# Optimization experiments

Measured on AMD Instinct MI355X. Metric: run time of the kernel, lower is better.

Reference implementation:

```python
import jax, jax.numpy as jnp
import numpy as np

N_FULL, N_LOCAL, N_GLOBAL = 6, 4, 2
N_HEADS = N_FULL + N_LOCAL + N_GLOBAL
WINDOW = 64
DIM = 1536
B, S = 2, 2048


def setup_inputs() -> dict:
    key = jax.random.key(0)
    k0, k1, k2 = jax.random.split(key, 3)
    sc = DIM ** -0.5
    return {
        "x": jax.random.normal(k0, (B, S, DIM), dtype=jnp.float32),
        "Wqkv": jax.random.normal(k1, (DIM, 3 * DIM), dtype=jnp.float32) * sc,
        "bqkv": jnp.zeros((3 * DIM,), dtype=jnp.float32),
        "Wout": jax.random.normal(k2, (DIM, DIM), dtype=jnp.float32) * sc,
        "bout": jnp.zeros((DIM,), dtype=jnp.float32),
    }


def _attend(q, k, v, scale, bias=None):
    # q,k,v: [B,H,S,D]
    scores = jnp.einsum("bhqd,bhkd->bhqk", q, k) * scale
    if bias is not None:
        scores = scores + bias
    p = jax.nn.softmax(scores, axis=-1)
    return jnp.einsum("bhqk,bhkd->bhqd", p, v)


def reference(x, Wqkv, bqkv, Wout, bout):
    Bb, Ss, D = x.shape
    hd = D // N_HEADS
    scale = hd ** -0.5
    qkv = (x @ Wqkv + bqkv).reshape(Bb, Ss, 3, N_HEADS, hd)
    qkv = jnp.transpose(qkv, (2, 0, 3, 1, 4))  # [3,B,H,S,hd]
    q, k, v = qkv[0], qkv[1], qkv[2]
    h1 = N_FULL
    h2 = N_FULL + N_LOCAL

    # tier 1: full attention on first n_full heads
    out_full = _attend(q[:, :h1], k[:, :h1], v[:, :h1], scale)

    # tier 2: sliding-window (|i-j| <= window//2 allowed) on next n_local heads
    idx = jnp.arange(Ss)
    allowed = jnp.abs(idx[:, None] - idx[None, :]) <= WINDOW // 2  # [S,S]
    bias = jnp.where(allowed, 0.0, -jnp.inf).astype(x.dtype)[None, None]
    out_local = _attend(q[:, h1:h2], k[:, h1:h2], v[:, h1:h2], scale, bias)

    # tier 3: global — attend only to first and last tokens
    kg = jnp.stack([k[:, h2:, 0], k[:, h2:, -1]], axis=2)  # [B,Hg,2,hd]
    vg = jnp.stack([v[:, h2:, 0], v[:, h2:, -1]], axis=2)
    out_global = _attend(q[:, h2:], kg, vg, scale)

    out = jnp.concatenate([out_full, out_local, out_global], axis=1)  # [B,H,S,hd]
    out = jnp.transpose(out, (0, 2, 1, 3)).reshape(Bb, Ss, D)
    return out @ Wout + bout
```

## Files before the change

### kernel.cpp

```cpp
#include <hip/hip_runtime.h>
#include <hip/hip_bf16.h>

#define SEQ    2048
#define TOK    4096
#define DMODEL 1536
#define QKVROW 4608
#define HD     128
#define SCALE  0.08838834764831845f

#define NSPLIT 4
#define KRANGE (SEQ / NSPLIT)
#define NPAIR  12
#define ROWS_P (NPAIR * SEQ)
#define OPART_ELEMS ((size_t)ROWS_P * HD)

typedef __attribute__((ext_vector_type(8))) short short8;
typedef __attribute__((ext_vector_type(4))) short short4v;
typedef __attribute__((ext_vector_type(4))) float f32x4;

__device__ __forceinline__ float b2f(short s) {
    union { unsigned u; float f; } x;
    x.u = ((unsigned)(unsigned short)s) << 16;
    return x.f;
}
__device__ __forceinline__ short f2b(float f) {
    union { float f; unsigned u; } x; x.f = f;
    unsigned u = x.u;
    unsigned r = (u + 0x7fffu + ((u >> 16) & 1u)) >> 16;
    return (short)r;
}

__device__ __forceinline__ void gld_lds16(const short* g, short* l) {
    __builtin_amdgcn_global_load_lds(
        (__attribute__((address_space(1))) void*)(g),
        (__attribute__((address_space(3))) void*)(l), 16, 0, 0);
}

#define CVT_BLOCKS  6144
#define TQKV_BLOCKS 1728
#define TOUT_BLOCKS 576

__device__ __forceinline__ void transpose_tile(
    const float* __restrict__ W, short* __restrict__ WT,
    int K, int N, int k0, int n0, int t, short (*tile)[65])
{
    {
        int j  = t & 63;
        int i0 = (t >> 6) * 16;
        for (int ii = 0; ii < 16; ++ii)
            tile[i0 + ii][j] = f2b(W[(size_t)(k0 + i0 + ii) * N + n0 + j]);
    }
    __syncthreads();
    {
        int i  = t & 63;
        int j0 = (t >> 6) * 16;
        for (int jj = 0; jj < 16; ++jj)
            WT[(size_t)(n0 + j0 + jj) * K + k0 + i] = tile[i][j0 + jj];
    }
}

__global__ __launch_bounds__(256) void prepass_k(
    const float* __restrict__ x, const float* __restrict__ Wqkv,
    const float* __restrict__ Wout, short* __restrict__ xb,
    short* __restrict__ WqkvT, short* __restrict__ WoutT)
{
    __shared__ short tile[64][65];
    const int bid = blockIdx.x;
    const int t   = threadIdx.x;
    if (bid < CVT_BLOCKS) {
        int i = bid * 1024 + t * 4;
        float4 v = *(const float4*)(x + i);
        short4v b = { f2b(v.x), f2b(v.y), f2b(v.z), f2b(v.w) };
        *(short4v*)(xb + i) = b;
    } else if (bid < CVT_BLOCKS + TQKV_BLOCKS) {
        int tb = bid - CVT_BLOCKS;
        transpose_tile(Wqkv, WqkvT, DMODEL, QKVROW,
                       (tb / (QKVROW / 64)) * 64, (tb % (QKVROW / 64)) * 64, t, tile);
    } else {
        int tb = bid - (CVT_BLOCKS + TQKV_BLOCKS);
        transpose_tile(Wout, WoutT, DMODEL, DMODEL,
                       (tb / (DMODEL / 64)) * 64, (tb % (DMODEL / 64)) * 64, t, tile);
    }
}

__device__ __forceinline__ short* ldsA(short* s, int slot, int kh, int st) {
    return s + ((slot * 2 + kh) * 8 + st) * 512;
}
__device__ __forceinline__ short* ldsB(short* s, int slot, int kh, int st) {
    return s + 16384 + ((slot * 2 + kh) * 16 + st) * 512;
}

template <int SLOT, int KH, int G>
__device__ __forceinline__ void ld_a(short8 af[2], short* smem, int wm4, int lane) {
#pragma unroll
    for (int mi = 0; mi < 2; ++mi)
        af[mi] = *(const short8*)(ldsA(smem, SLOT, KH, wm4 + G * 2 + mi) + lane * 8);
}
template <int SLOT, int KH>
__device__ __forceinline__ void ld_b(short8 bf[4], short* smem, int wn4, int lane) {
#pragma unroll
    for (int ni = 0; ni < 4; ++ni)
        bf[ni] = *(const short8*)(ldsB(smem, SLOT, KH, wn4 + ni) + lane * 8);
}
template <int G>
__device__ __forceinline__ void mfma8(f32x4 (&acc)[4][4], const short8 af[2], const short8 bf[4]) {
#pragma unroll
    for (int mi = 0; mi < 2; ++mi)
#pragma unroll
        for (int ni = 0; ni < 4; ++ni)
            acc[G * 2 + mi][ni] = __builtin_amdgcn_mfma_f32_16x16x32_bf16(
                af[mi], bf[ni], acc[G * 2 + mi][ni], 0, 0, 0);
}

#define STG_A(S, KH, KT) gld_lds16(gA0 + (KT) * 64 + (KH) * 32, ldsA(smem, (S), (KH), wave))
#define STG_B(S, KH, KT)                                                        \
    do {                                                                        \
        gld_lds16(gB0 + (KT) * 64 + (KH) * 32, ldsB(smem, (S), (KH), wave));    \
        gld_lds16(gB1 + (KT) * 64 + (KH) * 32, ldsB(smem, (S), (KH), 8 + wave));\
    } while (0)

#define PH(S, KH, G, LOADB, STG_STMT, VMW)                          \
    do {                                                            \
        ld_a<S, KH, G>(af, smem, wm4, lane);                        \
        if (LOADB) ld_b<S, KH>(bf, smem, wn4, lane);                \
        STG_STMT;                                                   \
        asm volatile("" ::: "memory");                              \
        __builtin_amdgcn_s_barrier();                               \
        asm volatile("s_waitcnt lgkmcnt(0)" ::: "memory");          \
        __builtin_amdgcn_s_setprio(1);                              \
        mfma8<G>(acc, af, bf);                                      \
        __builtin_amdgcn_s_setprio(0);                              \
        if (VMW) asm volatile("s_waitcnt vmcnt(5)" ::: "memory");   \
        asm volatile("" ::: "memory");                              \
        __builtin_amdgcn_s_barrier();                               \
        asm volatile("" ::: "memory");                              \
    } while (0)

template <bool OUT_BF16, int MT, int NT>
__global__ __launch_bounds__(512, 2) void gemm128x256_8ph(
    const short* __restrict__ A, const short* __restrict__ BT,
    const float* __restrict__ bias, void* __restrict__ Cout,
    int N, int K)
{
    __shared__ short smem[49152];

    constexpr int NWG = MT * NT;
    constexpr int Q8  = NWG / 8, R8 = NWG % 8;
    constexpr int BW  = 4;
    constexpr int FULLB = NT / BW;
    constexpr int TB  = FULLB * MT * BW;
    constexpr int TW  = NT - FULLB * BW;
    const int orig = blockIdx.x;
    const int xcd  = orig & 7, idx = orig >> 3;
    const int wg   = (xcd < R8 ? xcd * (Q8 + 1) : R8 * (Q8 + 1) + (xcd - R8) * Q8) + idx;
    int mt, nt;
    if (TW == 0 || wg < TB) {
        int band = wg / (MT * BW);
        int rem  = wg % (MT * BW);
        mt = rem / BW;
        nt = band * BW + rem % BW;
    } else {
        constexpr int TWD = TW ? TW : 1;
        int rem = wg - TB;
        mt = rem / TWD;
        nt = FULLB * BW + rem % TWD;
    }
    const int bm0 = mt * 128;
    const int bn0 = nt * 256;

    const int t    = threadIdx.x;
    const int wave = t >> 6;
    const int lane = t & 63;
    const int quad = lane >> 4;
    const int lo   = lane & 15;
    const int wm   = wave >> 2;
    const int wn   = wave & 3;
    const int wm4  = wm * 4;
    const int wn4  = wn * 4;

    const int rO = quad * 8;
    const short* gA0 = A  + (size_t)(bm0 + wave * 16 + lo) * K + rO;
    const short* gB0 = BT + (size_t)(bn0 + wave * 16 + lo) * K + rO;
    const short* gB1 = BT + (size_t)(bn0 + (8 + wave) * 16 + lo) * K + rO;

    f32x4 acc[4][4];
#pragma unroll
    for (int i = 0; i < 4; ++i)
#pragma unroll
        for (int j = 0; j < 4; ++j)
            acc[i][j] = (f32x4){0.f, 0.f, 0.f, 0.f};

    const int NTK = K >> 6;

    STG_A(0, 0, 0); STG_A(0, 1, 0); STG_B(0, 0, 0); STG_B(0, 1, 0);
    STG_B(1, 0, 1); STG_A(1, 0, 1); STG_B(1, 1, 1);
    asm volatile("s_waitcnt vmcnt(5)" ::: "memory");
    asm volatile("" ::: "memory");
    __builtin_amdgcn_s_barrier();
    asm volatile("" ::: "memory");

    short8 af[2], bf[4];
#pragma unroll 1
    for (int it = 0; it < (NTK >> 1); ++it) {
        const int T  = it * 2;
        const int t2 = min(T + 2, NTK - 1);
        const int t3 = min(T + 3, NTK - 1);
        PH(0, 0, 0, true,  STG_A(1, 1, T + 1), 0);
        PH(0, 0, 1, false, STG_B(0, 0, t2),    0);
        PH(0, 1, 0, true,  STG_A(0, 0, t2),    0);
        PH(0, 1, 1, false, STG_B(0, 1, t2),    1);
        PH(1, 0, 0, true,  STG_A(0, 1, t2),    0);
        PH(1, 0, 1, false, STG_B(1, 0, t3),    0);
        PH(1, 1, 0, true,  STG_A(1, 0, t3),    0);
        PH(1, 1, 1, false, STG_B(1, 1, t3),    1);
    }
    asm volatile("s_waitcnt vmcnt(0)" ::: "memory");

#pragma unroll
    for (int ni = 0; ni < 4; ++ni) {
        int col  = bn0 + wn * 64 + ni * 16 + lo;
        float bv = bias[col];
#pragma unroll
        for (int mi = 0; mi < 4; ++mi)
#pragma unroll
            for (int r = 0; r < 4; ++r) {
                int row   = bm0 + wm * 64 + mi * 16 + quad * 4 + r;
                float val = acc[mi][ni][r] + bv;
                if (OUT_BF16)
                    ((short*)Cout)[(size_t)row * N + col] = f2b(val);
                else
                    ((float*)Cout)[(size_t)row * N + col] = val;
            }
    }
}

#define KSP 136
#define VTP 44
#define PLP 40

__global__ __launch_bounds__(256) void attn_full_split(
    const short* __restrict__ qkv, short* __restrict__ Opart,
    float* __restrict__ lsum)
{
    const int pair = blockIdx.y;
    const int b    = pair / 6;
    const int h    = pair % 6;
    const int q0   = blockIdx.x * 64;
    const int kz   = blockIdx.z;
    const int t    = threadIdx.x;
    const int wave = t >> 6;
    const int lane = t & 63;
    const int quad = lane >> 4;
    const int lo   = lane & 15;

    __shared__ short Ks[32 * KSP];
    __shared__ short Vr[32 * KSP];
    __shared__ short Vt[128 * VTP];
    __shared__ short Pl[4][16 * PLP];

    const short* base = qkv + (size_t)b * SEQ * QKVROW;

    short8 qf[4];
    {
        int qrow = q0 + wave * 16 + lo;
        const short* qp = base + (size_t)qrow * QKVROW + h * HD;
        for (int c = 0; c < 4; ++c)
            qf[c] = *(const short8*)(qp + c * 32 + quad * 8);
    }

    f32x4 o[8];
    for (int i = 0; i < 8; ++i) o[i] = (f32x4){0.f, 0.f, 0.f, 0.f};
    float lrow[4] = {0.f, 0.f, 0.f, 0.f};

    const int skey = t >> 3;
    const int sdc  = (t & 7) * 16;
    const int thd  = t & 127;
    const int tkc  = (t >> 7) * 16;

    const int kend = kz * KRANGE + KRANGE;
    for (int k0 = kz * KRANGE; k0 < kend; k0 += 32) {
        {
            const short* kro = base + (size_t)(k0 + skey) * QKVROW + DMODEL     + h * HD + sdc;
            const short* vro = base + (size_t)(k0 + skey) * QKVROW + 2 * DMODEL + h * HD + sdc;
            short8 ka = *(const short8*)kro;
            short8 kb = *(const short8*)(kro + 8);
            short8 va = *(const short8*)vro;
            short8 vb = *(const short8*)(vro + 8);
            *(short8*)(Ks + skey * KSP + sdc)     = ka;
            *(short8*)(Ks + skey * KSP + sdc + 8) = kb;
            *(short8*)(Vr + skey * KSP + sdc)     = va;
            *(short8*)(Vr + skey * KSP + sdc + 8) = vb;
        }
        __syncthreads();

        {
            short8 x0, x1;
            for (int j = 0; j < 8; ++j) x0[j] = Vr[(tkc + j) * KSP + thd];
            for (int j = 0; j < 8; ++j) x1[j] = Vr[(tkc + 8 + j) * KSP + thd];
            *(short8*)(Vt + thd * VTP + tkc)     = x0;
            *(short8*)(Vt + thd * VTP + tkc + 8) = x1;
        }

        f32x4 s[2];
        s[0] = (f32x4){0.f, 0.f, 0.f, 0.f};
        s[1] = (f32x4){0.f, 0.f, 0.f, 0.f};
        for (int g = 0; g < 2; ++g)
            for (int c = 0; c < 4; ++c) {
                short8 kf = *(const short8*)(Ks + (g * 16 + lo) * KSP + c * 32 + quad * 8);
                s[g] = __builtin_amdgcn_mfma_f32_16x16x32_bf16(qf[c], kf, s[g], 0, 0, 0);
            }

        for (int g = 0; g < 2; ++g)
            for (int r = 0; r < 4; ++r) {
                float p = __expf(s[g][r] * SCALE);
                lrow[r] += p;
                Pl[wave][(quad * 4 + r) * PLP + g * 16 + lo] = f2b(p);
            }
        __syncthreads();

        short8 pf = *(const short8*)(&Pl[wave][lo * PLP + quad * 8]);
        for (int ni = 0; ni < 8; ++ni) {
            short8 vf = *(const short8*)(Vt + (ni * 16 + lo) * VTP + quad * 8);
            o[ni] = __builtin_amdgcn_mfma_f32_16x16x32_bf16(pf, vf, o[ni], 0, 0, 0);
        }
    }

    for (int r = 0; r < 4; ++r)
        for (int off = 1; off < 16; off <<= 1)
            lrow[r] += __shfl_xor(lrow[r], off, 64);

    for (int ni = 0; ni < 8; ++ni)
        for (int r = 0; r < 4; ++r) {
            int grow = pair * SEQ + q0 + wave * 16 + quad * 4 + r;
            Opart[(size_t)kz * OPART_ELEMS + (size_t)grow * HD + ni * 16 + lo] =
                f2b(o[ni][r]);
        }
    if (lo == 0)
        for (int r = 0; r < 4; ++r) {
            int grow = pair * SEQ + q0 + wave * 16 + quad * 4 + r;
            lsum[kz * ROWS_P + grow] = lrow[r];
        }
}

__global__ __launch_bounds__(256) void attn_local_mfma(
    const short* __restrict__ qkv, short* __restrict__ att)
{
    const int pair = blockIdx.y;
    const int b    = pair >> 2;
    const int h    = 6 + (pair & 3);
    const int q0   = blockIdx.x * 64;
    const int t    = threadIdx.x;
    const int wave = t >> 6;
    const int lane = t & 63;
    const int quad = lane >> 4;
    const int lo   = lane & 15;

    __shared__ short Ks[32 * KSP];
    __shared__ short Vr[32 * KSP];
    __shared__ short Vt[128 * VTP];
    __shared__ short Pl[4][16 * PLP];

    const short* base = qkv + (size_t)b * SEQ * QKVROW;

    short8 qf[4];
    {
        int qrow = q0 + wave * 16 + lo;
        const short* qp = base + (size_t)qrow * QKVROW + h * HD;
        for (int c = 0; c < 4; ++c)
            qf[c] = *(const short8*)(qp + c * 32 + quad * 8);
    }

    f32x4 o[8];
    for (int i = 0; i < 8; ++i) o[i] = (f32x4){0.f, 0.f, 0.f, 0.f};
    float lrow[4] = {0.f, 0.f, 0.f, 0.f};

    const int skey = t >> 3;
    const int sdc  = (t & 7) * 16;
    const int thd  = t & 127;
    const int tkc  = (t >> 7) * 16;
    const int irow = q0 + wave * 16 + quad * 4;

    const int ks = max(0, q0 - 32);
    const int ke = min(SEQ, q0 + 96);
    for (int k0 = ks; k0 < ke; k0 += 32) {
        {
            const short* kro = base + (size_t)(k0 + skey) * QKVROW + DMODEL     + h * HD + sdc;
            const short* vro = base + (size_t)(k0 + skey) * QKVROW + 2 * DMODEL + h * HD + sdc;
            short8 ka = *(const short8*)kro;
            short8 kb = *(const short8*)(kro + 8);
            short8 va = *(const short8*)vro;
            short8 vb = *(const short8*)(vro + 8);
            *(short8*)(Ks + skey * KSP + sdc)     = ka;
            *(short8*)(Ks + skey * KSP + sdc + 8) = kb;
            *(short8*)(Vr + skey * KSP + sdc)     = va;
            *(short8*)(Vr + skey * KSP + sdc + 8) = vb;
        }
        __syncthreads();

        {
            short8 x0, x1;
            for (int j = 0; j < 8; ++j) x0[j] = Vr[(tkc + j) * KSP + thd];
            for (int j = 0; j < 8; ++j) x1[j] = Vr[(tkc + 8 + j) * KSP + thd];
            *(short8*)(Vt + thd * VTP + tkc)     = x0;
            *(short8*)(Vt + thd * VTP + tkc + 8) = x1;
        }

        f32x4 s[2];
        s[0] = (f32x4){0.f, 0.f, 0.f, 0.f};
        s[1] = (f32x4){0.f, 0.f, 0.f, 0.f};
        for (int g = 0; g < 2; ++g)
            for (int c = 0; c < 4; ++c) {
                short8 kf = *(const short8*)(Ks + (g * 16 + lo) * KSP + c * 32 + quad * 8);
                s[g] = __builtin_amdgcn_mfma_f32_16x16x32_bf16(qf[c], kf, s[g], 0, 0, 0);
            }

        for (int g = 0; g < 2; ++g)
            for (int r = 0; r < 4; ++r) {
                int j = k0 + g * 16 + lo;
                int d = irow + r - j;
                float p = (d >= -32 && d <= 32) ? __expf(s[g][r] * SCALE) : 0.f;
                lrow[r] += p;
                Pl[wave][(quad * 4 + r) * PLP + g * 16 + lo] = f2b(p);
            }
        __syncthreads();

        short8 pf = *(const short8*)(&Pl[wave][lo * PLP + quad * 8]);
        for (int ni = 0; ni < 8; ++ni) {
            short8 vf = *(const short8*)(Vt + (ni * 16 + lo) * VTP + quad * 8);
            o[ni] = __builtin_amdgcn_mfma_f32_16x16x32_bf16(pf, vf, o[ni], 0, 0, 0);
        }
    }

    for (int r = 0; r < 4; ++r)
        for (int off = 1; off < 16; off <<= 1)
            lrow[r] += __shfl_xor(lrow[r], off, 64);

    for (int ni = 0; ni < 8; ++ni)
        for (int r = 0; r < 4; ++r) {
            int row = irow + r;
            size_t off = ((size_t)(b * SEQ + row)) * DMODEL + h * HD + ni * 16 + lo;
            att[off] = f2b(o[ni][r] / lrow[r]);
        }
}

#define MERGE_BLOCKS  12288
#define GLOBAL_BLOCKS 2048

__global__ __launch_bounds__(256) void postattn_k(
    const short* __restrict__ qkv, const short* __restrict__ Opart,
    const float* __restrict__ lsum, short* __restrict__ att)
{
    const int bid  = blockIdx.x;
    const int t    = threadIdx.x;
    const int wave = t >> 6;
    const int lane = t & 63;

    if (bid < MERGE_BLOCKS) {
        int idx  = bid * 256 + t;
        int pair = idx >> 18;
        int q    = (idx >> 7) & (SEQ - 1);
        int hd   = idx & (HD - 1);
        int row  = pair * SEQ + q;
        float osum = 0.f, ls = 0.f;
        for (int z = 0; z < NSPLIT; ++z) {
            ls   += lsum[z * ROWS_P + row];
            osum += b2f(Opart[(size_t)z * OPART_ELEMS + (size_t)row * HD + hd]);
        }
        int b = pair / 6, h = pair % 6;
        att[((size_t)(b * SEQ + q)) * DMODEL + h * HD + hd] = f2b(osum / ls);
    } else {
        int gb   = bid - MERGE_BLOCKS;
        int pair = gb >> 9;
        int q    = (gb & 511) * 4 + wave;
        int b    = pair >> 1;
        int h    = 10 + (pair & 1);

        const short* base = qkv + (size_t)b * SEQ * QKVROW;
        const short* qp   = base + (size_t)q * QKVROW + h * HD;
        const short* k0   = base + DMODEL + h * HD;
        const short* k1   = base + (size_t)(SEQ - 1) * QKVROW + DMODEL + h * HD;

        float s0 = fmaf(b2f(qp[lane]), b2f(k0[lane]),
                   b2f(qp[lane + 64]) * b2f(k0[lane + 64]));
        float s1 = fmaf(b2f(qp[lane]), b2f(k1[lane]),
                   b2f(qp[lane + 64]) * b2f(k1[lane + 64]));
        for (int off = 1; off < 64; off <<= 1) {
            s0 += __shfl_xor(s0, off, 64);
            s1 += __shfl_xor(s1, off, 64);
        }
        s0 *= SCALE; s1 *= SCALE;
        float m  = fmaxf(s0, s1);
        float e0 = __expf(s0 - m), e1 = __expf(s1 - m);
        float inv = 1.f / (e0 + e1);
        float p0 = e0 * inv, p1 = e1 * inv;

        const short* v0 = base + 2 * DMODEL + h * HD;
        const short* v1 = base + (size_t)(SEQ - 1) * QKVROW + 2 * DMODEL + h * HD;
        size_t ob = ((size_t)(b * SEQ + q)) * DMODEL + h * HD;
        att[ob + lane]      = f2b(fmaf(p0, b2f(v0[lane]),      p1 * b2f(v1[lane])));
        att[ob + lane + 64] = f2b(fmaf(p0, b2f(v0[lane + 64]), p1 * b2f(v1[lane + 64])));
    }
}

extern "C" void kernel_launch(void* const* d_in, const int* in_sizes, int n_in,
                              void* d_out, int out_size, void* d_ws, size_t ws_size,
                              hipStream_t stream) {
    const float* x    = (const float*)d_in[0];
    const float* Wqkv = (const float*)d_in[1];
    const float* bqkv = (const float*)d_in[2];
    const float* Wout = (const float*)d_in[3];
    const float* bout = (const float*)d_in[4];

    char* p = (char*)d_ws;
    short* qkv   = (short*)p;  p += (size_t)TOK * QKVROW * 2;
    short* Opart = (short*)p;  p += OPART_ELEMS * NSPLIT * 2;
    float* lsum  = (float*)p;  p += (size_t)ROWS_P * NSPLIT * 4;
    short* xb    = (short*)p;  p += (size_t)TOK * DMODEL * 2;
    short* att   = xb;
    short* WqkvT = (short*)p;  p += (size_t)QKVROW * DMODEL * 2;
    short* WoutT = (short*)p;

    prepass_k<<<dim3(CVT_BLOCKS + TQKV_BLOCKS + TOUT_BLOCKS), 256, 0, stream>>>(
        x, Wqkv, Wout, xb, WqkvT, WoutT);
    gemm128x256_8ph<true, 32, 18><<<dim3(32 * 18), 512, 0, stream>>>(
        xb, WqkvT, bqkv, (void*)qkv, QKVROW, DMODEL);
    attn_full_split<<<dim3(SEQ / 64, NPAIR, NSPLIT), 256, 0, stream>>>(qkv, Opart, lsum);
    attn_local_mfma<<<dim3(SEQ / 64, 8), 256, 0, stream>>>(qkv, att);
    postattn_k<<<dim3(MERGE_BLOCKS + GLOBAL_BLOCKS), 256, 0, stream>>>(
        qkv, Opart, lsum, att);
    gemm128x256_8ph<false, 32, 6><<<dim3(32 * 6), 512, 0, stream>>>(
        att, WoutT, bout, d_out, DMODEL, DMODEL);
}
```

Before: 336.8 us.

## Use 256x256 tiles for QKV GEMM and drop pre-MFMA barrier

Templates the 8-phase GEMM on the M-fragment count so the QKV projection uses 256x256 workgroup tiles (MF=4), while the output projection keeps 128x256. Larger tiles double the reuse of the B operand from LDS and global memory and halve the number of workgroups. The change also removes the per-phase barrier and explicit LDS wait that sat between the fragment loads and the MFMAs, trimming synchronisation. In exchange, LDS grows to 128KB and the accumulators to 128 floats per lane, which lowers occupancy. With only 288 workgroups the tail may be poorly balanced across CUs.

Result: no change. 337.7 us (+0.2%).

```diff
diff --git a/kernel.cpp b/kernel.cpp
--- a/kernel.cpp
+++ b/kernel.cpp
@@ -83,66 +83,79 @@
     }
 }
 
+template <int MF>
 __device__ __forceinline__ short* ldsA(short* s, int slot, int kh, int st) {
-    return s + ((slot * 2 + kh) * 8 + st) * 512;
-}
+    return s + ((slot * 2 + kh) * (4 * MF) + st) * 512;
+}
+template <int MF>
 __device__ __forceinline__ short* ldsB(short* s, int slot, int kh, int st) {
-    return s + 16384 + ((slot * 2 + kh) * 16 + st) * 512;
-}
-
-template <int SLOT, int KH, int G>
-__device__ __forceinline__ void ld_a(short8 af[2], short* smem, int wm4, int lane) {
-#pragma unroll
-    for (int mi = 0; mi < 2; ++mi)
-        af[mi] = *(const short8*)(ldsA(smem, SLOT, KH, wm4 + G * 2 + mi) + lane * 8);
-}
-template <int SLOT, int KH>
-__device__ __forceinline__ void ld_b(short8 bf[4], short* smem, int wn4, int lane) {
+    return s + 8192 * MF + ((slot * 2 + kh) * 16 + st) * 512;
+}
+
+template <int MF, int SLOT, int KH, int G>
+__device__ __forceinline__ void ld_a(short8* af, short* smem, int wm, int lane) {
+#pragma unroll
+    for (int mi = 0; mi < MF; ++mi)
+        af[mi] = *(const short8*)(
+            ldsA<MF>(smem, SLOT, KH, wm * 2 * MF + G * MF + mi) + lane * 8);
+}
+template <int MF, int SLOT, int KH>
+__device__ __forceinline__ void ld_b(short8* bf, short* smem, int wn4, int lane) {
 #pragma unroll
     for (int ni = 0; ni < 4; ++ni)
-        bf[ni] = *(const short8*)(ldsB(smem, SLOT, KH, wn4 + ni) + lane * 8);
-}
-template <int G>
-__device__ __forceinline__ void mfma8(f32x4 (&acc)[4][4], const short8 af[2], const short8 bf[4]) {
-#pragma unroll
-    for (int mi = 0; mi < 2; ++mi)
+        bf[ni] = *(const short8*)(ldsB<MF>(smem, SLOT, KH, wn4 + ni) + lane * 8);
+}
+template <int MF, int G>
+__device__ __forceinline__ void mfmaG(f32x4 (&acc)[2 * MF][4],
+                                      const short8* af, const short8* bf) {
+#pragma unroll
+    for (int mi = 0; mi < MF; ++mi)
 #pragma unroll
         for (int ni = 0; ni < 4; ++ni)
-            acc[G * 2 + mi][ni] = __builtin_amdgcn_mfma_f32_16x16x32_bf16(
-                af[mi], bf[ni], acc[G * 2 + mi][ni], 0, 0, 0);
-}
-
-#define STG_A(S, KH, KT) gld_lds16(gA0 + (KT) * 64 + (KH) * 32, ldsA(smem, (S), (KH), wave))
-#define STG_B(S, KH, KT)                                                        \
-    do {                                                                        \
-        gld_lds16(gB0 + (KT) * 64 + (KH) * 32, ldsB(smem, (S), (KH), wave));    \
-        gld_lds16(gB1 + (KT) * 64 + (KH) * 32, ldsB(smem, (S), (KH), 8 + wave));\
+            acc[G * MF + mi][ni] = __builtin_amdgcn_mfma_f32_16x16x32_bf16(
+                af[mi], bf[ni], acc[G * MF + mi][ni], 0, 0, 0);
+}
+template <int MF>
+__device__ __forceinline__ void vmwait() {
+    if constexpr (MF == 4) asm volatile("s_waitcnt vmcnt(6)" ::: "memory");
+    else                   asm volatile("s_waitcnt vmcnt(5)" ::: "memory");
+}
+
+#define STG_A(S, KH, KT)                                                          \
+    do {                                                                          \
+        gld_lds16(gA0 + (KT) * 64 + (KH) * 32, ldsA<MF_>(smem, (S), (KH), wave)); \
+        if constexpr (MF_ == 4)                                                   \
+            gld_lds16(gA1 + (KT) * 64 + (KH) * 32,                                \
+                      ldsA<MF_>(smem, (S), (KH), 8 + wave));                      \
+    } while (0)
+#define STG_B(S, KH, KT)                                                          \
+    do {                                                                          \
+        gld_lds16(gB0 + (KT) * 64 + (KH) * 32, ldsB<MF_>(smem, (S), (KH), wave)); \
+        gld_lds16(gB1 + (KT) * 64 + (KH) * 32,                                    \
+                  ldsB<MF_>(smem, (S), (KH), 8 + wave));                          \
     } while (0)
 
 #define PH(S, KH, G, LOADB, STG_STMT, VMW)                          \
     do {                                                            \
-        ld_a<S, KH, G>(af, smem, wm4, lane);                        \
-        if (LOADB) ld_b<S, KH>(bf, smem, wn4, lane);                \
+        ld_a<MF_, S, KH, G>(af, smem, wm, lane);                    \
+        if (LOADB) ld_b<MF_, S, KH>(bf, smem, wn4, lane);           \
         STG_STMT;                                                   \
-        asm volatile("" ::: "memory");                              \
-        __builtin_amdgcn_s_barrier();                               \
-        asm volatile("s_waitcnt lgkmcnt(0)" ::: "memory");          \
         __builtin_amdgcn_s_setprio(1);                              \
-        mfma8<G>(acc, af, bf);                                      \
+        mfmaG<MF_, G>(acc, af, bf);                                 \
         __builtin_amdgcn_s_setprio(0);                              \
-        if (VMW) asm volatile("s_waitcnt vmcnt(5)" ::: "memory");   \
+        if (VMW) vmwait<MF_>();                                     \
         asm volatile("" ::: "memory");                              \
         __builtin_amdgcn_s_barrier();                               \
         asm volatile("" ::: "memory");                              \
     } while (0)
 
-template <bool OUT_BF16, int MT, int NT>
-__global__ __launch_bounds__(512, 2) void gemm128x256_8ph(
+template <bool OUT_BF16, int MF_, int MT, int NT>
+__global__ __launch_bounds__(512, 2) void gemm_8ph(
     const short* __restrict__ A, const short* __restrict__ BT,
     const float* __restrict__ bias, void* __restrict__ Cout,
     int N, int K)
 {
-    __shared__ short smem[49152];
+    __shared__ short smem[8192 * MF_ + 32768];
 
     constexpr int NWG = MT * NT;
     constexpr int Q8  = NWG / 8, R8 = NWG % 8;
@@ -165,7 +178,7 @@
         mt = rem / TWD;
         nt = FULLB * BW + rem % TWD;
     }
-    const int bm0 = mt * 128;
+    const int bm0 = mt * (64 * MF_);
     const int bn0 = nt * 256;
 
     const int t    = threadIdx.x;
@@ -175,17 +188,17 @@
     const int lo   = lane & 15;
     const int wm   = wave >> 2;
     const int wn   = wave & 3;
-    const int wm4  = wm * 4;
     const int wn4  = wn * 4;
 
     const int rO = quad * 8;
     const short* gA0 = A  + (size_t)(bm0 + wave * 16 + lo) * K + rO;
+    const short* gA1 = A  + (size_t)(bm0 + (8 + wave) * 16 + lo) * K + rO;
     const short* gB0 = BT + (size_t)(bn0 + wave * 16 + lo) * K + rO;
     const short* gB1 = BT + (size_t)(bn0 + (8 + wave) * 16 + lo) * K + rO;
 
-    f32x4 acc[4][4];
-#pragma unroll
-    for (int i = 0; i < 4; ++i)
+    f32x4 acc[2 * MF_][4];
+#pragma unroll
+    for (int i = 0; i < 2 * MF_; ++i)
 #pragma unroll
         for (int j = 0; j < 4; ++j)
             acc[i][j] = (f32x4){0.f, 0.f, 0.f, 0.f};
@@ -194,12 +207,12 @@
 
     STG_A(0, 0, 0); STG_A(0, 1, 0); STG_B(0, 0, 0); STG_B(0, 1, 0);
     STG_B(1, 0, 1); STG_A(1, 0, 1); STG_B(1, 1, 1);
-    asm volatile("s_waitcnt vmcnt(5)" ::: "memory");
+    vmwait<MF_>();
     asm volatile("" ::: "memory");
     __builtin_amdgcn_s_barrier();
     asm volatile("" ::: "memory");
 
-    short8 af[2], bf[4];
+    short8 af[MF_], bf[4];
 #pragma unroll 1
     for (int it = 0; it < (NTK >> 1); ++it) {
         const int T  = it * 2;
@@ -221,11 +234,11 @@
         int col  = bn0 + wn * 64 + ni * 16 + lo;
         float bv = bias[col];
 #pragma unroll
-        for (int mi = 0; mi < 4; ++mi)
+        for (int a = 0; a < 2 * MF_; ++a)
 #pragma unroll
             for (int r = 0; r < 4; ++r) {
-                int row   = bm0 + wm * 64 + mi * 16 + quad * 4 + r;
-                float val = acc[mi][ni][r] + bv;
+                int row   = bm0 + wm * 32 * MF_ + a * 16 + quad * 4 + r;
+                float val = acc[a][ni][r] + bv;
                 if (OUT_BF16)
                     ((short*)Cout)[(size_t)row * N + col] = f2b(val);
                 else
@@ -522,12 +535,12 @@
 
     prepass_k<<<dim3(CVT_BLOCKS + TQKV_BLOCKS + TOUT_BLOCKS), 256, 0, stream>>>(
         x, Wqkv, Wout, xb, WqkvT, WoutT);
-    gemm128x256_8ph<true, 32, 18><<<dim3(32 * 18), 512, 0, stream>>>(
+    gemm_8ph<true, 4, 16, 18><<<dim3(16 * 18), 512, 0, stream>>>(
         xb, WqkvT, bqkv, (void*)qkv, QKVROW, DMODEL);
     attn_full_split<<<dim3(SEQ / 64, NPAIR, NSPLIT), 256, 0, stream>>>(qkv, Opart, lsum);
     attn_local_mfma<<<dim3(SEQ / 64, 8), 256, 0, stream>>>(qkv, att);
     postattn_k<<<dim3(MERGE_BLOCKS + GLOBAL_BLOCKS), 256, 0, stream>>>(
         qkv, Opart, lsum, att);
-    gemm128x256_8ph<false, 32, 6><<<dim3(32 * 6), 512, 0, stream>>>(
+    gemm_8ph<false, 2, 32, 6><<<dim3(32 * 6), 512, 0, stream>>>(
         att, WoutT, bout, d_out, DMODEL, DMODEL);
 }
```

## Replace 8-phase GEMM pipeline with simpler 2-phase double buffer at K=32

Applied to the files above, without the earlier changes.

The GEMM main loop changes from an 8-phase schedule with 64-wide K tiles and staggered partial-tile prefetches to a 2-stage double buffer over 32-wide K tiles. Each stage waits vmcnt(0) before its barrier. Shared memory per block is halved and launch bounds are raised to allow 4 blocks per CU, trading finer latency hiding for higher occupancy. The full wait on global loads each half-iteration may expose memory latency, and 512-thread blocks with 4 per CU may be limited by registers.

Result: slower. 353.1 us (+4.8%).

```diff
diff --git a/kernel.cpp b/kernel.cpp
--- a/kernel.cpp
+++ b/kernel.cpp
@@ -83,66 +83,46 @@
     }
 }
 
-__device__ __forceinline__ short* ldsA(short* s, int slot, int kh, int st) {
-    return s + ((slot * 2 + kh) * 8 + st) * 512;
-}
-__device__ __forceinline__ short* ldsB(short* s, int slot, int kh, int st) {
-    return s + 16384 + ((slot * 2 + kh) * 16 + st) * 512;
-}
-
-template <int SLOT, int KH, int G>
-__device__ __forceinline__ void ld_a(short8 af[2], short* smem, int wm4, int lane) {
-#pragma unroll
-    for (int mi = 0; mi < 2; ++mi)
-        af[mi] = *(const short8*)(ldsA(smem, SLOT, KH, wm4 + G * 2 + mi) + lane * 8);
-}
-template <int SLOT, int KH>
-__device__ __forceinline__ void ld_b(short8 bf[4], short* smem, int wn4, int lane) {
-#pragma unroll
-    for (int ni = 0; ni < 4; ++ni)
-        bf[ni] = *(const short8*)(ldsB(smem, SLOT, KH, wn4 + ni) + lane * 8);
-}
-template <int G>
-__device__ __forceinline__ void mfma8(f32x4 (&acc)[4][4], const short8 af[2], const short8 bf[4]) {
-#pragma unroll
-    for (int mi = 0; mi < 2; ++mi)
-#pragma unroll
-        for (int ni = 0; ni < 4; ++ni)
-            acc[G * 2 + mi][ni] = __builtin_amdgcn_mfma_f32_16x16x32_bf16(
-                af[mi], bf[ni], acc[G * 2 + mi][ni], 0, 0, 0);
-}
-
-#define STG_A(S, KH, KT) gld_lds16(gA0 + (KT) * 64 + (KH) * 32, ldsA(smem, (S), (KH), wave))
-#define STG_B(S, KH, KT)                                                        \
-    do {                                                                        \
-        gld_lds16(gB0 + (KT) * 64 + (KH) * 32, ldsB(smem, (S), (KH), wave));    \
-        gld_lds16(gB1 + (KT) * 64 + (KH) * 32, ldsB(smem, (S), (KH), 8 + wave));\
+#define LD_A(S, G)                                                            \
+    do {                                                                      \
+        af[0] = *(const short8*)(smem + ((S) * 8 + wm * 4 + (G) * 2) * 512 + lane * 8); \
+        af[1] = *(const short8*)(smem + ((S) * 8 + wm * 4 + (G) * 2 + 1) * 512 + lane * 8); \
     } while (0)
-
-#define PH(S, KH, G, LOADB, STG_STMT, VMW)                          \
-    do {                                                            \
-        ld_a<S, KH, G>(af, smem, wm4, lane);                        \
-        if (LOADB) ld_b<S, KH>(bf, smem, wn4, lane);                \
-        STG_STMT;                                                   \
-        asm volatile("" ::: "memory");                              \
-        __builtin_amdgcn_s_barrier();                               \
-        asm volatile("s_waitcnt lgkmcnt(0)" ::: "memory");          \
-        __builtin_amdgcn_s_setprio(1);                              \
-        mfma8<G>(acc, af, bf);                                      \
-        __builtin_amdgcn_s_setprio(0);                              \
-        if (VMW) asm volatile("s_waitcnt vmcnt(5)" ::: "memory");   \
-        asm volatile("" ::: "memory");                              \
-        __builtin_amdgcn_s_barrier();                               \
-        asm volatile("" ::: "memory");                              \
+#define LD_B(S)                                                               \
+    do {                                                                      \
+        for (int ni = 0; ni < 4; ++ni)                                        \
+            bf[ni] = *(const short8*)(smem + 8192 + ((S) * 16 + wn4 + ni) * 512 + lane * 8); \
     } while (0)
+#define MFMA_G(G)                                                             \
+    do {                                                                      \
+        __builtin_amdgcn_s_setprio(1);                                        \
+        for (int mi = 0; mi < 2; ++mi)                                        \
+            for (int ni = 0; ni < 4; ++ni)                                    \
+                acc[(G) * 2 + mi][ni] = __builtin_amdgcn_mfma_f32_16x16x32_bf16( \
+                    af[mi], bf[ni], acc[(G) * 2 + mi][ni], 0, 0, 0);          \
+        __builtin_amdgcn_s_setprio(0);                                        \
+    } while (0)
+#define STG(S, KT)                                                            \
+    do {                                                                      \
+        gld_lds16(gA0 + (KT) * 32, smem + ((S) * 8 + wave) * 512);            \
+        gld_lds16(gB0 + (KT) * 32, smem + 8192 + ((S) * 16 + wave) * 512);    \
+        gld_lds16(gB1 + (KT) * 32, smem + 8192 + ((S) * 16 + 8 + wave) * 512);\
+    } while (0)
+#define BAR                                                                   \
+    do {                                                                      \
+        asm volatile("" ::: "memory");                                        \
+        __builtin_amdgcn_s_barrier();                                         \
+        asm volatile("" ::: "memory");                                        \
+    } while (0)
+#define VM0 asm volatile("s_waitcnt vmcnt(0)" ::: "memory")
 
 template <bool OUT_BF16, int MT, int NT>
-__global__ __launch_bounds__(512, 2) void gemm128x256_8ph(
+__global__ __launch_bounds__(512, 4) void gemm_2ph(
     const short* __restrict__ A, const short* __restrict__ BT,
     const float* __restrict__ bias, void* __restrict__ Cout,
     int N, int K)
 {
-    __shared__ short smem[49152];
+    __shared__ short smem[24576];
 
     constexpr int NWG = MT * NT;
     constexpr int Q8  = NWG / 8, R8 = NWG % 8;
@@ -175,7 +155,6 @@
     const int lo   = lane & 15;
     const int wm   = wave >> 2;
     const int wn   = wave & 3;
-    const int wm4  = wm * 4;
     const int wn4  = wn * 4;
 
     const int rO = quad * 8;
@@ -190,42 +169,45 @@
         for (int j = 0; j < 4; ++j)
             acc[i][j] = (f32x4){0.f, 0.f, 0.f, 0.f};
 
-    const int NTK = K >> 6;
-
-    STG_A(0, 0, 0); STG_A(0, 1, 0); STG_B(0, 0, 0); STG_B(0, 1, 0);
-    STG_B(1, 0, 1); STG_A(1, 0, 1); STG_B(1, 1, 1);
-    asm volatile("s_waitcnt vmcnt(5)" ::: "memory");
-    asm volatile("" ::: "memory");
-    __builtin_amdgcn_s_barrier();
-    asm volatile("" ::: "memory");
+    const int NTK = K >> 5;
+
+    STG(0, 0);
+    VM0;
+    BAR;
 
     short8 af[2], bf[4];
 #pragma unroll 1
     for (int it = 0; it < (NTK >> 1); ++it) {
-        const int T  = it * 2;
-        const int t2 = min(T + 2, NTK - 1);
-        const int t3 = min(T + 3, NTK - 1);
-        PH(0, 0, 0, true,  STG_A(1, 1, T + 1), 0);
-        PH(0, 0, 1, false, STG_B(0, 0, t2),    0);
-        PH(0, 1, 0, true,  STG_A(0, 0, t2),    0);
-        PH(0, 1, 1, false, STG_B(0, 1, t2),    1);
-        PH(1, 0, 0, true,  STG_A(0, 1, t2),    0);
-        PH(1, 0, 1, false, STG_B(1, 0, t3),    0);
-        PH(1, 1, 0, true,  STG_A(1, 0, t3),    0);
-        PH(1, 1, 1, false, STG_B(1, 1, t3),    1);
-    }
-    asm volatile("s_waitcnt vmcnt(0)" ::: "memory");
+        const int t1 = 2 * it + 1;
+        const int t2 = min(2 * it + 2, NTK - 1);
+        LD_B(0); LD_A(0, 0);
+        STG(1, t1);
+        MFMA_G(0);
+        BAR;
+        LD_A(0, 1);
+        MFMA_G(1);
+        VM0;
+        BAR;
+        LD_B(1); LD_A(1, 0);
+        STG(0, t2);
+        MFMA_G(0);
+        BAR;
+        LD_A(1, 1);
+        MFMA_G(1);
+        VM0;
+        BAR;
+    }
 
 #pragma unroll
     for (int ni = 0; ni < 4; ++ni) {
         int col  = bn0 + wn * 64 + ni * 16 + lo;
         float bv = bias[col];
 #pragma unroll
-        for (int mi = 0; mi < 4; ++mi)
+        for (int a = 0; a < 4; ++a)
 #pragma unroll
             for (int r = 0; r < 4; ++r) {
-                int row   = bm0 + wm * 64 + mi * 16 + quad * 4 + r;
-                float val = acc[mi][ni][r] + bv;
+                int row   = bm0 + wm * 64 + a * 16 + quad * 4 + r;
+                float val = acc[a][ni][r] + bv;
                 if (OUT_BF16)
                     ((short*)Cout)[(size_t)row * N + col] = f2b(val);
                 else
@@ -522,12 +504,12 @@
 
     prepass_k<<<dim3(CVT_BLOCKS + TQKV_BLOCKS + TOUT_BLOCKS), 256, 0, stream>>>(
         x, Wqkv, Wout, xb, WqkvT, WoutT);
-    gemm128x256_8ph<true, 32, 18><<<dim3(32 * 18), 512, 0, stream>>>(
+    gemm_2ph<true, 32, 18><<<dim3(32 * 18), 512, 0, stream>>>(
         xb, WqkvT, bqkv, (void*)qkv, QKVROW, DMODEL);
     attn_full_split<<<dim3(SEQ / 64, NPAIR, NSPLIT), 256, 0, stream>>>(qkv, Opart, lsum);
     attn_local_mfma<<<dim3(SEQ / 64, 8), 256, 0, stream>>>(qkv, att);
     postattn_k<<<dim3(MERGE_BLOCKS + GLOBAL_BLOCKS), 256, 0, stream>>>(
         qkv, Opart, lsum, att);
-    gemm128x256_8ph<false, 32, 6><<<dim3(32 * 6), 512, 0, stream>>>(
+    gemm_2ph<false, 32, 6><<<dim3(32 * 6), 512, 0, stream>>>(
         att, WoutT, bout, d_out, DMODEL, DMODEL);
 }
```
